# Performance work log

Hardware: AMD Instinct MI355X
Metric: run time of the kernel (lower is better)

## Reference

```python
import jax, jax.numpy as jnp
import numpy as np

N_PATCH, N_Z, K, BS = 16, 128, 10, 1024
D = N_PATCH * N_Z


def setup_inputs() -> dict:
    key = jax.random.key(0)
    k1, k2, k3, k4 = jax.random.split(key, 4)
    z = jax.random.normal(k1, (BS, D), dtype=jnp.float32)
    m = jax.random.normal(k2, (K, D), dtype=jnp.float32)
    L = jax.random.normal(k3, (K, D, D), dtype=jnp.float32)
    components = jax.random.randint(k4, (BS,), 0, K, dtype=jnp.int64)
    return {"z": z, "m": m, "L": L, "components": components}


def reference(z, m, L, components):
    # samps[k] = m[k] + z @ L[k].T   -> (K, BS, D)
    samps = jnp.einsum('bd,ked->kbe', z, L) + m[:, None, :]
    # one-hot mask-and-sum over components == gather selected expert per sample
    x = samps[components, jnp.arange(z.shape[0])]  # (BS, D)
    return x.reshape(-1, N_PATCH, N_Z)
```

## Files before the change

### kernel.cpp

```cpp
#include <hip/hip_runtime.h>
#include <hip/hip_bf16.h>


#define DDIM  2048
#define BSAMP 1024
#define KCOMP 10
#define MPAD  160
#define NT    32
#define BK    32
#define NITER (DDIM / BK)
#define TILEB (MPAD * BK * 2)
#define ABYTES TILEB
#define BBYTES (NT * BK * 4)
#define STAGE_BYTES (ABYTES + BBYTES)

typedef __attribute__((ext_vector_type(8))) short bf16x8;
typedef __attribute__((ext_vector_type(4))) float f32x4;

__device__ __forceinline__ void async16(void* lds, const void* g) {
    __builtin_amdgcn_global_load_lds(
        (const __attribute__((address_space(1))) void*)g,
        (__attribute__((address_space(3))) void*)lds, 16, 0, 0);
}

__device__ __forceinline__ short bfs(float x) {
    __hip_bfloat16 h = __float2bfloat16(x);
    return *reinterpret_cast<short*>(&h);
}

__global__ void build_map(const int* __restrict__ comp,
                          int* __restrict__ rowmap,
                          int* __restrict__ counts) {
    __shared__ int sc[KCOMP];
    const int t = threadIdx.x;
    if (t < KCOMP) sc[t] = 0;
    __syncthreads();
    const int c = comp[t];
    const int r = atomicAdd(&sc[c], 1);
    if (r < MPAD) rowmap[c * MPAD + r] = t;
    __syncthreads();
    if (t < KCOMP) counts[t] = sc[t];
}

__global__ void zgather(const float* __restrict__ z,
                        const int* __restrict__ rowmap,
                        short* __restrict__ zb) {
    const int k  = blockIdx.x;
    const int sp = blockIdx.y;
    const int t  = threadIdx.x;
    const int c  = t & 7;
    const int g  = c & 3;
    const int s0 = rowmap[k * MPAD + 2 * sp]     & (BSAMP - 1);
    const int s1 = rowmap[k * MPAD + 2 * sp + 1] & (BSAMP - 1);
    const int src = (c >> 2) ? s1 : s0;
    const int swz = (c ^ (sp & 7)) * 16;
    char* kbase = (char*)zb + (size_t)k * NITER * TILEB + sp * 128 + swz;
#pragma unroll
    for (int p = 0; p < 2; ++p) {
        const int it = p * 32 + (t >> 3);
        const float* zr = z + (size_t)src * DDIM + it * BK + g * 8;
        f32x4 x = *(const f32x4*)zr;
        f32x4 y = *(const f32x4*)(zr + 4);
        bf16x8 r;
#pragma unroll
        for (int i = 0; i < 4; ++i) { r[i] = bfs(x[i]); r[4 + i] = bfs(y[i]); }
        *(bf16x8*)(kbase + (size_t)it * TILEB) = r;
    }
}

__global__ __launch_bounds__(256, 4)
void gmm_gemm(const short* __restrict__ zb,
              const float* __restrict__ mvec,
              const float* __restrict__ Lmat,
              const int* __restrict__ rowmap,
              const int* __restrict__ counts,
              float* __restrict__ out) {
    __shared__ __attribute__((aligned(16))) char smem[2 * STAGE_BYTES];
    const int t    = threadIdx.x;
    const int lane = t & 63;
    const int w    = t >> 6;
    const int mh   = w >> 1;
    const int nh   = w & 1;
    const int k    = blockIdx.y;
    const int n0   = blockIdx.x * NT;
    const float* Lk = Lmat + (size_t)k * DDIM * DDIM;
    const char* zt  = (const char*)zb + (size_t)k * NITER * TILEB;
    const int cnt  = counts[k];

    int mtmax = (cnt - mh * 80 + 15) >> 4;
    mtmax = mtmax < 0 ? 0 : (mtmax > 5 ? 5 : mtmax);

    const int br = t >> 3,          bc = ((t & 7) ^ (br & 7)) * 4;
    const unsigned ub = (unsigned)(t & ~63) * 16;

    auto stage = [&](int buf, int it) {
        char* lb = smem + buf * STAGE_BYTES;
        const char* at = zt + (size_t)it * TILEB;
        async16(lb + ub,        at + t * 16);
        async16(lb + 4096 + ub, at + 4096 + t * 16);
        if (t < 128)
            async16(lb + 8192 + ub, at + 8192 + t * 16);
        async16(lb + ABYTES + ub,
                Lk + (size_t)(n0 + br) * DDIM + it * BK + bc);
    };

    f32x4 acc[5];
#pragma unroll
    for (int mt = 0; mt < 5; ++mt) acc[mt] = (f32x4){0.f, 0.f, 0.f, 0.f};

    stage(0, 0);
    __syncthreads();

    const int fr = lane & 15;
    const int g  = lane >> 4;
    const int rb = nh * 16 + fr;
    const int h0 = ((2 * g)     ^ (rb & 7)) * 4;
    const int h1 = ((2 * g + 1) ^ (rb & 7)) * 4;
    const int frh = fr >> 1;
    const int fra = (fr & 1) * 4 + g;
    const int abase = (mh * 40 + frh) * 128 + ((fra ^ frh) * 16);

    for (int it = 0; it < NITER; ++it) {
        if (it + 1 < NITER) stage((it + 1) & 1, it + 1);
        const char* lb = smem + (it & 1) * STAGE_BYTES;
        const float* B = (const float*)(lb + ABYTES);

        f32x4 x = *(const f32x4*)(B + rb * 32 + h0);
        f32x4 y = *(const f32x4*)(B + rb * 32 + h1);
        bf16x8 bb;
#pragma unroll
        for (int i = 0; i < 4; ++i) { bb[i] = bfs(x[i]); bb[4 + i] = bfs(y[i]); }

#pragma unroll
        for (int mt = 0; mt < 5; ++mt) {
            if (mt < mtmax) {
                bf16x8 a = *(const bf16x8*)(lb + abase + mt * 1024);
                acc[mt] = __builtin_amdgcn_mfma_f32_16x16x32_bf16(a, bb, acc[mt], 0, 0, 0);
            }
        }
        __syncthreads();
    }

    const int rquad = g * 4;
    const int e  = n0 + nh * 16 + fr;
    const float mu = mvec[k * DDIM + e];
#pragma unroll
    for (int mt = 0; mt < 5; ++mt) {
        if (mt < mtmax) {
            const int sb = mh * 80 + mt * 16 + rquad;
#pragma unroll
            for (int r = 0; r < 4; ++r) {
                const int slot = sb + r;
                if (slot < cnt) {
                    const int b = rowmap[k * MPAD + slot];
                    out[(size_t)b * DDIM + e] = acc[mt][r] + mu;
                }
            }
        }
    }
}

extern "C" void kernel_launch(void* const* d_in, const int* in_sizes, int n_in,
                              void* d_out, int out_size, void* d_ws, size_t ws_size,
                              hipStream_t stream) {
    const float* z    = (const float*)d_in[0];
    const float* mvec = (const float*)d_in[1];
    const float* Lmat = (const float*)d_in[2];
    const int* comp   = (const int*)d_in[3];
    float* out        = (float*)d_out;

    int* rowmap = (int*)d_ws;
    int* counts = rowmap + KCOMP * MPAD;
    short* zb   = (short*)((char*)d_ws + 8192);

    build_map<<<1, BSAMP, 0, stream>>>(comp, rowmap, counts);
    zgather<<<dim3(KCOMP, MPAD / 2), 256, 0, stream>>>(z, rowmap, zb);
    gmm_gemm<<<dim3(DDIM / NT, KCOMP), 256, 0, stream>>>(zb, mvec, Lmat,
                                                         rowmap, counts, out);
}
```

Before: 269.5 us.

## Triple-buffer GEMM LDS stages with explicit vmcnt waits

The grouped GEMM moves from a double-buffered loop with a full __syncthreads per iteration to a three-stage LDS ring. It is driven by explicit s_waitcnt vmcnt counts and raw s_barrier calls, so two tiles of L and z stay in flight while the current one is consumed. To keep the per-thread load count uniform for vmcnt accounting, the z tile stride is padded to 12288 bytes and every thread now issues the third A load. This adds extra workspace and redundant loads of unused padding rows. The larger LDS footprint lowers launch bounds from 4 to 3 blocks per SM, trading occupancy for deeper latency hiding.

```diff
diff --git a/kernel.cpp b/kernel.cpp
--- a/kernel.cpp
+++ b/kernel.cpp
@@ -9,10 +9,11 @@
 #define NT    32
 #define BK    32
 #define NITER (DDIM / BK)
-#define TILEB (MPAD * BK * 2)
-#define ABYTES TILEB
-#define BBYTES (NT * BK * 4)
+#define TILEP 12288
+#define ABYTES 12288
+#define BBYTES 4096
 #define STAGE_BYTES (ABYTES + BBYTES)
+#define NBUF  3
 
 typedef __attribute__((ext_vector_type(8))) short bf16x8;
 typedef __attribute__((ext_vector_type(4))) float f32x4;
@@ -54,7 +55,7 @@
     const int s1 = rowmap[k * MPAD + 2 * sp + 1] & (BSAMP - 1);
     const int src = (c >> 2) ? s1 : s0;
     const int swz = (c ^ (sp & 7)) * 16;
-    char* kbase = (char*)zb + (size_t)k * NITER * TILEB + sp * 128 + swz;
+    char* kbase = (char*)zb + (size_t)k * NITER * TILEP + sp * 128 + swz;
 #pragma unroll
     for (int p = 0; p < 2; ++p) {
         const int it = p * 32 + (t >> 3);
@@ -64,18 +65,18 @@
         bf16x8 r;
 #pragma unroll
         for (int i = 0; i < 4; ++i) { r[i] = bfs(x[i]); r[4 + i] = bfs(y[i]); }
-        *(bf16x8*)(kbase + (size_t)it * TILEB) = r;
+        *(bf16x8*)(kbase + (size_t)it * TILEP) = r;
     }
 }
 
-__global__ __launch_bounds__(256, 4)
+__global__ __launch_bounds__(256, 3)
 void gmm_gemm(const short* __restrict__ zb,
               const float* __restrict__ mvec,
               const float* __restrict__ Lmat,
               const int* __restrict__ rowmap,
               const int* __restrict__ counts,
               float* __restrict__ out) {
-    __shared__ __attribute__((aligned(16))) char smem[2 * STAGE_BYTES];
+    __shared__ __attribute__((aligned(16))) char smem[NBUF * STAGE_BYTES];
     const int t    = threadIdx.x;
     const int lane = t & 63;
     const int w    = t >> 6;
@@ -84,7 +85,7 @@
     const int k    = blockIdx.y;
     const int n0   = blockIdx.x * NT;
     const float* Lk = Lmat + (size_t)k * DDIM * DDIM;
-    const char* zt  = (const char*)zb + (size_t)k * NITER * TILEB;
+    const char* zt  = (const char*)zb + (size_t)k * NITER * TILEP;
     const int cnt  = counts[k];
 
     int mtmax = (cnt - mh * 80 + 15) >> 4;
@@ -93,23 +94,18 @@
     const int br = t >> 3,          bc = ((t & 7) ^ (br & 7)) * 4;
     const unsigned ub = (unsigned)(t & ~63) * 16;
 
-    auto stage = [&](int buf, int it) {
-        char* lb = smem + buf * STAGE_BYTES;
-        const char* at = zt + (size_t)it * TILEB;
-        async16(lb + ub,        at + t * 16);
-        async16(lb + 4096 + ub, at + 4096 + t * 16);
-        if (t < 128)
-            async16(lb + 8192 + ub, at + 8192 + t * 16);
-        async16(lb + ABYTES + ub,
-                Lk + (size_t)(n0 + br) * DDIM + it * BK + bc);
+    auto stage = [&](int bi, int it) {
+        char* lb = smem + bi * STAGE_BYTES;
+        const char* at = zt + (size_t)it * TILEP;
+        async16(lb + ub,          at + t * 16);
+        async16(lb + 4096 + ub,   at + 4096 + t * 16);
+        async16(lb + 8192 + ub,   at + 8192 + t * 16);
+        async16(lb + ABYTES + ub, Lk + (size_t)(n0 + br) * DDIM + it * BK + bc);
     };
 
     f32x4 acc[5];
 #pragma unroll
     for (int mt = 0; mt < 5; ++mt) acc[mt] = (f32x4){0.f, 0.f, 0.f, 0.f};
-
-    stage(0, 0);
-    __syncthreads();
 
     const int fr = lane & 15;
     const int g  = lane >> 4;
@@ -120,17 +116,14 @@
     const int fra = (fr & 1) * 4 + g;
     const int abase = (mh * 40 + frh) * 128 + ((fra ^ frh) * 16);
 
-    for (int it = 0; it < NITER; ++it) {
-        if (it + 1 < NITER) stage((it + 1) & 1, it + 1);
-        const char* lb = smem + (it & 1) * STAGE_BYTES;
+    auto compute = [&](int bi) {
+        const char* lb = smem + bi * STAGE_BYTES;
         const float* B = (const float*)(lb + ABYTES);
-
         f32x4 x = *(const f32x4*)(B + rb * 32 + h0);
         f32x4 y = *(const f32x4*)(B + rb * 32 + h1);
         bf16x8 bb;
 #pragma unroll
         for (int i = 0; i < 4; ++i) { bb[i] = bfs(x[i]); bb[4 + i] = bfs(y[i]); }
-
 #pragma unroll
         for (int mt = 0; mt < 5; ++mt) {
             if (mt < mtmax) {
@@ -138,8 +131,26 @@
                 acc[mt] = __builtin_amdgcn_mfma_f32_16x16x32_bf16(a, bb, acc[mt], 0, 0, 0);
             }
         }
-        __syncthreads();
+    };
+
+    stage(0, 0); stage(1, 1); stage(2, 2);
+    int bi = 0;
+    for (int it = 0; it < NITER - 2; ++it) {
+        asm volatile("s_waitcnt vmcnt(8)" ::: "memory");
+        __builtin_amdgcn_s_barrier();
+        compute(bi);
+        __builtin_amdgcn_s_barrier();
+        if (it + 3 < NITER) stage(bi, it + 3);
+        bi = (bi == NBUF - 1) ? 0 : bi + 1;
     }
+    asm volatile("s_waitcnt vmcnt(4)" ::: "memory");
+    __builtin_amdgcn_s_barrier();
+    compute(bi);
+    __builtin_amdgcn_s_barrier();
+    bi = (bi == NBUF - 1) ? 0 : bi + 1;
+    asm volatile("s_waitcnt vmcnt(0)" ::: "memory");
+    __builtin_amdgcn_s_barrier();
+    compute(bi);
 
     const int rquad = g * 4;
     const int e  = n0 + nh * 16 + fr;
```

Result: no change. 271.3 us (+0.7%).

## Fuse map build, gather and GEMM into one cooperative kernel with grid syncs

Applied to the files above, without the earlier changes.

Merges the three launches (row-map build, z gather/convert, grouped GEMM) into a single cooperative kernel of 640 workgroups that uses grid-wide syncs between phases. A fallback keeps the three-kernel path if cooperative launch is unsupported or occupancy is too low. This targets the launch overhead and inter-kernel gaps, at the cost of two grid barriers and the serial single-block map-build phase inside the fused kernel.

```diff
diff --git a/kernel.cpp b/kernel.cpp
--- a/kernel.cpp
+++ b/kernel.cpp
@@ -1,6 +1,9 @@
 #include <hip/hip_runtime.h>
 #include <hip/hip_bf16.h>
-
+#include <hip/hip_cooperative_groups.h>
+
+
+namespace cg = cooperative_groups;
 
 #define DDIM  2048
 #define BSAMP 1024
@@ -9,10 +12,12 @@
 #define NT    32
 #define BK    32
 #define NITER (DDIM / BK)
-#define TILEB (MPAD * BK * 2)
+#define TILEB 10240
 #define ABYTES TILEB
-#define BBYTES (NT * BK * 4)
+#define BBYTES 4096
 #define STAGE_BYTES (ABYTES + BBYTES)
+#define NWG   (KCOMP * 64)
+#define ZUNITS (KCOMP * 80)
 
 typedef __attribute__((ext_vector_type(8))) short bf16x8;
 typedef __attribute__((ext_vector_type(4))) float f32x4;
@@ -28,26 +33,12 @@
     return *reinterpret_cast<short*>(&h);
 }
 
-__global__ void build_map(const int* __restrict__ comp,
-                          int* __restrict__ rowmap,
-                          int* __restrict__ counts) {
-    __shared__ int sc[KCOMP];
-    const int t = threadIdx.x;
-    if (t < KCOMP) sc[t] = 0;
-    __syncthreads();
-    const int c = comp[t];
-    const int r = atomicAdd(&sc[c], 1);
-    if (r < MPAD) rowmap[c * MPAD + r] = t;
-    __syncthreads();
-    if (t < KCOMP) counts[t] = sc[t];
-}
-
-__global__ void zgather(const float* __restrict__ z,
-                        const int* __restrict__ rowmap,
-                        short* __restrict__ zb) {
-    const int k  = blockIdx.x;
-    const int sp = blockIdx.y;
-    const int t  = threadIdx.x;
+__device__ __forceinline__ void zgather_unit(const float* __restrict__ z,
+                                             const int* __restrict__ rowmap,
+                                             short* __restrict__ zb,
+                                             int u, int t) {
+    const int k  = u / 80;
+    const int sp = u - k * 80;
     const int c  = t & 7;
     const int g  = c & 3;
     const int s0 = rowmap[k * MPAD + 2 * sp]     & (BSAMP - 1);
@@ -68,21 +59,18 @@
     }
 }
 
-__global__ __launch_bounds__(256, 4)
-void gmm_gemm(const short* __restrict__ zb,
-              const float* __restrict__ mvec,
-              const float* __restrict__ Lmat,
-              const int* __restrict__ rowmap,
-              const int* __restrict__ counts,
-              float* __restrict__ out) {
-    __shared__ __attribute__((aligned(16))) char smem[2 * STAGE_BYTES];
-    const int t    = threadIdx.x;
+__device__ __forceinline__ void gmm_body(char* smem,
+                                         const short* __restrict__ zb,
+                                         const float* __restrict__ mvec,
+                                         const float* __restrict__ Lmat,
+                                         const int* __restrict__ rowmap,
+                                         const int* __restrict__ counts,
+                                         float* __restrict__ out,
+                                         int k, int n0, int t) {
     const int lane = t & 63;
     const int w    = t >> 6;
     const int mh   = w >> 1;
     const int nh   = w & 1;
-    const int k    = blockIdx.y;
-    const int n0   = blockIdx.x * NT;
     const float* Lk = Lmat + (size_t)k * DDIM * DDIM;
     const char* zt  = (const char*)zb + (size_t)k * NITER * TILEB;
     const int cnt  = counts[k];
@@ -160,6 +148,76 @@
     }
 }
 
+__global__ __launch_bounds__(256, 3)
+void gmm_fused(const float* __restrict__ z,
+               const float* __restrict__ mvec,
+               const float* __restrict__ Lmat,
+               const int* __restrict__ comp,
+               int* __restrict__ rowmap,
+               int* __restrict__ counts,
+               short* __restrict__ zb,
+               float* __restrict__ out) {
+    __shared__ __attribute__((aligned(16))) char smem[2 * STAGE_BYTES];
+    const int t   = threadIdx.x;
+    const int bid = blockIdx.x;
+
+    if (bid == 0) {
+        __shared__ int sc[KCOMP];
+        if (t < KCOMP) sc[t] = 0;
+        __syncthreads();
+#pragma unroll
+        for (int j = 0; j < 4; ++j) {
+            const int i = j * 256 + t;
+            const int c = comp[i];
+            const int r = atomicAdd(&sc[c], 1);
+            if (r < MPAD) rowmap[c * MPAD + r] = i;
+        }
+        __syncthreads();
+        if (t < KCOMP) counts[t] = sc[t];
+    }
+    cg::this_grid().sync();
+
+    zgather_unit(z, rowmap, zb, bid, t);
+    if (bid < ZUNITS - NWG) zgather_unit(z, rowmap, zb, NWG + bid, t);
+    cg::this_grid().sync();
+
+    gmm_body(smem, zb, mvec, Lmat, rowmap, counts, out,
+             bid >> 6, (bid & 63) * NT, t);
+}
+
+__global__ void build_map_k(const int* __restrict__ comp,
+                            int* __restrict__ rowmap,
+                            int* __restrict__ counts) {
+    __shared__ int sc[KCOMP];
+    const int t = threadIdx.x;
+    if (t < KCOMP) sc[t] = 0;
+    __syncthreads();
+    const int c = comp[t];
+    const int r = atomicAdd(&sc[c], 1);
+    if (r < MPAD) rowmap[c * MPAD + r] = t;
+    __syncthreads();
+    if (t < KCOMP) counts[t] = sc[t];
+}
+
+__global__ void zgather_k(const float* __restrict__ z,
+                          const int* __restrict__ rowmap,
+                          short* __restrict__ zb) {
+    zgather_unit(z, rowmap, zb, blockIdx.x, threadIdx.x);
+}
+
+__global__ __launch_bounds__(256, 2)
+void gmm_k(const short* __restrict__ zb,
+           const float* __restrict__ mvec,
+           const float* __restrict__ Lmat,
+           const int* __restrict__ rowmap,
+           const int* __restrict__ counts,
+           float* __restrict__ out) {
+    __shared__ __attribute__((aligned(16))) char smem[2 * STAGE_BYTES];
+    gmm_body(smem, zb, mvec, Lmat, rowmap, counts, out,
+             (int)blockIdx.x >> 6, ((int)blockIdx.x & 63) * NT,
+             (int)threadIdx.x);
+}
+
 extern "C" void kernel_launch(void* const* d_in, const int* in_sizes, int n_in,
                               void* d_out, int out_size, void* d_ws, size_t ws_size,
                               hipStream_t stream) {
@@ -173,8 +231,26 @@
     int* counts = rowmap + KCOMP * MPAD;
     short* zb   = (short*)((char*)d_ws + 8192);
 
-    build_map<<<1, BSAMP, 0, stream>>>(comp, rowmap, counts);
-    zgather<<<dim3(KCOMP, MPAD / 2), 256, 0, stream>>>(z, rowmap, zb);
-    gmm_gemm<<<dim3(DDIM / NT, KCOMP), 256, 0, stream>>>(zb, mvec, Lmat,
-                                                         rowmap, counts, out);
-}
+    static int coop = -1;
+    if (coop < 0) {
+        hipDeviceProp_t prop{};
+        int dev = 0;
+        (void)hipGetDevice(&dev);
+        (void)hipGetDeviceProperties(&prop, dev);
+        int nb = 0;
+        (void)hipOccupancyMaxActiveBlocksPerMultiprocessor(&nb, gmm_fused, 256, 0);
+        coop = (prop.cooperativeLaunch &&
+                (long)nb * prop.multiProcessorCount >= NWG) ? 1 : 0;
+    }
+    if (coop) {
+        void* args[] = {(void*)&z, (void*)&mvec, (void*)&Lmat, (void*)&comp,
+                        (void*)&rowmap, (void*)&counts, (void*)&zb, (void*)&out};
+        if (hipLaunchCooperativeKernel(gmm_fused, dim3(NWG), dim3(256),
+                                       args, 0, stream) == hipSuccess)
+            return;
+        coop = 0;
+    }
+    build_map_k<<<1, BSAMP, 0, stream>>>(comp, rowmap, counts);
+    zgather_k<<<ZUNITS, 256, 0, stream>>>(z, rowmap, zb);
+    gmm_k<<<NWG, 256, 0, stream>>>(zb, mvec, Lmat, rowmap, counts, out);
+}
```

New measurement: 421.8 us. 56.5% more time.

## Split GEMM workgroups by M-half into 128-thread blocks, doubling grid size

Applied to the files above, without the earlier changes.

Each 256-thread workgroup that handled both 80-row halves of a component's padded sample tile becomes two 128-thread workgroups, one per M-half, launched as a flat grid of 1280 blocks. Each block stages only its half of the bf16 z tile plus the full 32-column fp32 L tile, which shrinks LDS per block and raises the number of resident waves and blocks. In exchange, every L column tile is now loaded from global memory twice (once per M-half), adding L traffic on an already bandwidth-heavy kernel, and each thread issues more async loads per stage.

```diff
diff --git a/kernel.cpp b/kernel.cpp
--- a/kernel.cpp
+++ b/kernel.cpp
@@ -9,10 +9,12 @@
 #define NT    32
 #define BK    32
 #define NITER (DDIM / BK)
-#define TILEB (MPAD * BK * 2)
-#define ABYTES TILEB
-#define BBYTES (NT * BK * 4)
-#define STAGE_BYTES (ABYTES + BBYTES)
+#define TILEB 10240
+#define AHALF 5120
+#define ALDSB 6144
+#define BBYTES 4096
+#define STAGE_BYTES (ALDSB + BBYTES)
+#define NWG   (KCOMP * 64 * 2)
 
 typedef __attribute__((ext_vector_type(8))) short bf16x8;
 typedef __attribute__((ext_vector_type(4))) float f32x4;
@@ -68,7 +70,7 @@
     }
 }
 
-__global__ __launch_bounds__(256, 4)
+__global__ __launch_bounds__(128, 4)
 void gmm_gemm(const short* __restrict__ zb,
               const float* __restrict__ mvec,
               const float* __restrict__ Lmat,
@@ -78,11 +80,11 @@
     __shared__ __attribute__((aligned(16))) char smem[2 * STAGE_BYTES];
     const int t    = threadIdx.x;
     const int lane = t & 63;
-    const int w    = t >> 6;
-    const int mh   = w >> 1;
-    const int nh   = w & 1;
-    const int k    = blockIdx.y;
-    const int n0   = blockIdx.x * NT;
+    const int nh   = t >> 6;
+    const int bid  = blockIdx.x;
+    const int mh   = bid & 1;
+    const int n0   = ((bid >> 1) & 63) * NT;
+    const int k    = bid >> 7;
     const float* Lk = Lmat + (size_t)k * DDIM * DDIM;
     const char* zt  = (const char*)zb + (size_t)k * NITER * TILEB;
     const int cnt  = counts[k];
@@ -90,18 +92,22 @@
     int mtmax = (cnt - mh * 80 + 15) >> 4;
     mtmax = mtmax < 0 ? 0 : (mtmax > 5 ? 5 : mtmax);
 
-    const int br = t >> 3,          bc = ((t & 7) ^ (br & 7)) * 4;
+    const int br0 = t >> 3,        bc0 = ((t & 7) ^ (br0 & 7)) * 4;
+    const int c1  = 128 + t;
+    const int br1 = c1 >> 3,       bc1 = ((c1 & 7) ^ (br1 & 7)) * 4;
+    const int ac2 = (256 + t < 320) ? (256 + t) : 319;
     const unsigned ub = (unsigned)(t & ~63) * 16;
 
     auto stage = [&](int buf, int it) {
         char* lb = smem + buf * STAGE_BYTES;
-        const char* at = zt + (size_t)it * TILEB;
-        async16(lb + ub,        at + t * 16);
-        async16(lb + 4096 + ub, at + 4096 + t * 16);
-        if (t < 128)
-            async16(lb + 8192 + ub, at + 8192 + t * 16);
-        async16(lb + ABYTES + ub,
-                Lk + (size_t)(n0 + br) * DDIM + it * BK + bc);
+        const char* at = zt + (size_t)it * TILEB + mh * AHALF;
+        async16(lb + ub,          at + t * 16);
+        async16(lb + 2048 + ub,   at + 2048 + t * 16);
+        async16(lb + 4096 + ub,   at + ac2 * 16);
+        async16(lb + ALDSB + ub,
+                Lk + (size_t)(n0 + br0) * DDIM + it * BK + bc0);
+        async16(lb + ALDSB + 2048 + ub,
+                Lk + (size_t)(n0 + br1) * DDIM + it * BK + bc1);
     };
 
     f32x4 acc[5];
@@ -118,12 +124,12 @@
     const int h1 = ((2 * g + 1) ^ (rb & 7)) * 4;
     const int frh = fr >> 1;
     const int fra = (fr & 1) * 4 + g;
-    const int abase = (mh * 40 + frh) * 128 + ((fra ^ frh) * 16);
+    const int abase = frh * 128 + ((fra ^ frh) * 16);
 
     for (int it = 0; it < NITER; ++it) {
         if (it + 1 < NITER) stage((it + 1) & 1, it + 1);
         const char* lb = smem + (it & 1) * STAGE_BYTES;
-        const float* B = (const float*)(lb + ABYTES);
+        const float* B = (const float*)(lb + ALDSB);
 
         f32x4 x = *(const f32x4*)(B + rb * 32 + h0);
         f32x4 y = *(const f32x4*)(B + rb * 32 + h1);
@@ -175,6 +181,5 @@
 
     build_map<<<1, BSAMP, 0, stream>>>(comp, rowmap, counts);
     zgather<<<dim3(KCOMP, MPAD / 2), 256, 0, stream>>>(z, rowmap, zb);
-    gmm_gemm<<<dim3(DDIM / NT, KCOMP), 256, 0, stream>>>(zb, mvec, Lmat,
-                                                         rowmap, counts, out);
+    gmm_gemm<<<NWG, 128, 0, stream>>>(zb, mvec, Lmat, rowmap, counts, out);
 }
```

New measurement: 280.6 us. +4.1%, slower.
